# Performance work log

Hardware: AMD Instinct MI355X
Metric: run time of the kernel (lower is better)

## Reference

```python
import jax, jax.numpy as jnp
import numpy as np

B, T, D_IN, D_MODEL = 16, 4096, 256, 128
LN_EPS = 1e-5


def setup_inputs() -> dict:
    key = jax.random.key(0)
    ks = jax.random.split(key, 8)
    s_in = 1.0 / np.sqrt(D_MODEL)  # torch GRU init scale (1/sqrt(hidden))
    x = jax.random.normal(ks[0], (B, T, D_IN), dtype=jnp.float32)
    w_ih = jax.random.uniform(ks[1], (3 * D_MODEL, D_IN), minval=-s_in, maxval=s_in, dtype=jnp.float32)
    w_hh = jax.random.uniform(ks[2], (3 * D_MODEL, D_MODEL), minval=-s_in, maxval=s_in, dtype=jnp.float32)
    b_ih = jax.random.uniform(ks[3], (3 * D_MODEL,), minval=-s_in, maxval=s_in, dtype=jnp.float32)
    b_hh = jax.random.uniform(ks[4], (3 * D_MODEL,), minval=-s_in, maxval=s_in, dtype=jnp.float32)
    w_proj = jax.random.uniform(ks[5], (D_MODEL, D_MODEL), minval=-s_in, maxval=s_in, dtype=jnp.float32)
    b_proj = jax.random.uniform(ks[6], (D_MODEL,), minval=-s_in, maxval=s_in, dtype=jnp.float32)
    gamma = jnp.ones((D_MODEL,), dtype=jnp.float32)
    beta = jnp.zeros((D_MODEL,), dtype=jnp.float32)
    return {"x": x, "w_ih": w_ih, "w_hh": w_hh, "b_ih": b_ih, "b_hh": b_hh,
            "w_proj": w_proj, "b_proj": b_proj, "gamma": gamma, "beta": beta}


def _gru_scan(x, w_ih, w_hh, b_ih, b_hh):
    # x: [B,T,D_in]; precompute input-gate GEMM for all timesteps at once
    gi_all = jnp.einsum('btd,gd->btg', x, w_ih) + b_ih  # [B,T,3H]
    H = w_hh.shape[1]

    def step(h, gi):
        gh = h @ w_hh.T + b_hh                     # [B,3H]
        ir, iz, inn = jnp.split(gi, 3, axis=-1)    # torch gate order: r, z, n
        hr, hz, hn = jnp.split(gh, 3, axis=-1)
        r = jax.nn.sigmoid(ir + hr)
        z = jax.nn.sigmoid(iz + hz)
        n = jnp.tanh(inn + r * hn)
        h_new = (1.0 - z) * n + z * h
        return h_new, h_new

    h0 = jnp.zeros((x.shape[0], H), dtype=x.dtype)
    _, hs = jax.lax.scan(step, h0, jnp.swapaxes(gi_all, 0, 1))  # [T,B,H]
    return jnp.swapaxes(hs, 0, 1)                               # [B,T,H]


def reference(x, w_ih, w_hh, b_ih, b_hh, w_proj, b_proj, gamma, beta):
    out = _gru_scan(x, w_ih, w_hh, b_ih, b_hh)        # GRU output [B,T,H]
    y = out @ w_proj.T + b_proj                        # Linear(d_model, d_model)
    mu = jnp.mean(y, axis=-1, keepdims=True)
    var = jnp.mean(jnp.square(y - mu), axis=-1, keepdims=True)
    return (y - mu) * jax.lax.rsqrt(var + LN_EPS) * gamma + beta
```

## Files before the change

### kernel.cpp

```cpp
#include <hip/hip_runtime.h>
#include <hip/hip_fp16.h>

#define B_   16
#define T_   4096
#define DIN  256
#define H_   128
#define G3   384

#define SC_RZ 1.4426950408889634f
#define SC_N  2.8853900817779268f

typedef _Float16 half2_t __attribute__((ext_vector_type(2)));

__device__ __forceinline__ float fdot2(unsigned int a, unsigned int b, float c) {
#if __has_builtin(__builtin_amdgcn_fdot2)
  return __builtin_amdgcn_fdot2(__builtin_bit_cast(half2_t, a),
                                __builtin_bit_cast(half2_t, b), c, false);
#else
  const __half2 ha = __builtin_bit_cast(__half2, a);
  const __half2 hb = __builtin_bit_cast(__half2, b);
  return c + __half2float(__low2half(ha)) * __half2float(__low2half(hb))
           + __half2float(__high2half(ha)) * __half2float(__high2half(hb));
#endif
}

template <int CTRL>
__device__ __forceinline__ float dpp_xor_add(float x) {
  const int yi = __builtin_amdgcn_mov_dpp(__builtin_bit_cast(int, x),
                                          CTRL, 0xF, 0xF, true);
  return x + __builtin_bit_cast(float, yi);
}

__device__ __forceinline__ unsigned int pack2(float x, float y) {
  __half2 h = __floats2half2_rn(x, y);
  return __builtin_bit_cast(unsigned int, h);
}

__device__ __forceinline__ float fexp2(float x) {
#if __has_builtin(__builtin_amdgcn_exp2f)
  return __builtin_amdgcn_exp2f(x);
#else
  return exp2f(x);
#endif
}
__device__ __forceinline__ float frcp(float x) {
#if __has_builtin(__builtin_amdgcn_rcpf)
  return __builtin_amdgcn_rcpf(x);
#else
  return 1.f / x;
#endif
}

__device__ __forceinline__ void scan_barrier() {
  asm volatile("s_waitcnt lgkmcnt(0)" ::: "memory");
  __builtin_amdgcn_s_barrier();
  asm volatile("" ::: "memory");
}

__device__ __forceinline__ void barrier_lds() {
  asm volatile("s_waitcnt lgkmcnt(0)" ::: "memory");
  __builtin_amdgcn_s_barrier();
  asm volatile("" ::: "memory");
}

__device__ __forceinline__ void wave_lds_fence() {
  asm volatile("s_waitcnt lgkmcnt(0)" ::: "memory");
}

__global__ __launch_bounds__(384, 1) void gi_gemm(
    const float* __restrict__ x, const float* __restrict__ w_ih,
    const float* __restrict__ b_ih, const float* __restrict__ b_hh,
    __half* __restrict__ gi) {
  const int j = threadIdx.x;
  const int rbase = blockIdx.x * 128;

  __half2 wreg[128];
  const float* wrow = w_ih + (size_t)j * DIN;
#pragma unroll
  for (int k = 0; k < 128; ++k) {
    float2 w2 = reinterpret_cast<const float2*>(wrow)[k];
    wreg[k] = __floats2half2_rn(w2.x, w2.y);
  }
  const float bias = b_ih[j] + ((j < 256) ? b_hh[j] : 0.f);
  const __half2 z2h = __floats2half2_rn(0.f, 0.f);

  __shared__ alignas(16) unsigned int xs[16 * 128];

  for (int c = 0; c < 8; ++c) {
    barrier_lds();
    const int row0 = rbase + c * 16;
    for (int i = j; i < 16 * 128; i += 384) {
      const int r = i >> 7, col = i & 127;
      float2 v = reinterpret_cast<const float2*>(x + (size_t)(row0 + r) * DIN)[col];
      xs[i] = pack2(v.x, v.y);
    }
    barrier_lds();
    for (int r = 0; r < 16; ++r) {
      __half2 a0 = z2h, a1 = z2h, a2 = z2h, a3 = z2h;
      const uint4* hp = reinterpret_cast<const uint4*>(xs + r * 128);
#pragma unroll
      for (int k = 0; k < 32; ++k) {
        uint4 hv = hp[k];
        a0 = __hfma2(wreg[4 * k + 0], __builtin_bit_cast(__half2, hv.x), a0);
        a1 = __hfma2(wreg[4 * k + 1], __builtin_bit_cast(__half2, hv.y), a1);
        a2 = __hfma2(wreg[4 * k + 2], __builtin_bit_cast(__half2, hv.z), a2);
        a3 = __hfma2(wreg[4 * k + 3], __builtin_bit_cast(__half2, hv.w), a3);
      }
      const __half2 s2 = __hadd2(__hadd2(a0, a1), __hadd2(a2, a3));
      const float acc = bias + __low2float(s2) + __high2float(s2);
      gi[(size_t)(row0 + r) * G3 + j] = __float2half(acc);
    }
  }
}

__global__ __launch_bounds__(256, 1) void gru_scan(
    const __half* __restrict__ gi, const float* __restrict__ w_hh,
    const float* __restrict__ b_hh, float* __restrict__ out) {
  const int b   = blockIdx.x;
  const int tid = threadIdx.x;
  const int l   = tid & 63;
  const int w   = tid >> 6;
  const int half = l & 1;
  const int c   = w * 32 + (l >> 1);

  __half2 wgt[3][32];
#pragma unroll
  for (int g = 0; g < 3; ++g) {
    const float sg = (g < 2) ? -SC_RZ : -SC_N;
    const float* row = w_hh + (size_t)(g * H_ + c) * H_ + half * 64;
#pragma unroll
    for (int k = 0; k < 32; ++k) {
      float2 a = reinterpret_cast<const float2*>(row)[k];
      wgt[g][k] = __floats2half2_rn(a.x * sg, a.y * sg);
    }
  }
  const float bnS = b_hh[2 * H_ + c] * -SC_N;
  const __half2 initN = __floats2half2_rn((half == 0) ? bnS : 0.f, 0.f);
  const __half2 z2h = __floats2half2_rn(0.f, 0.f);

  __shared__ alignas(16) char hA[288];
  __shared__ alignas(16) char hB[288];
  if (tid < 72) reinterpret_cast<unsigned int*>(hA)[tid] = 0u;

  const int abase = half * 144;
  const int woff  = (c < 64) ? (c * 2) : (144 + (c - 64) * 2);

  const __half* gp = gi + (size_t)b * T_ * G3;
  float* po = out + ((size_t)b * T_) * H_ + c;
  const int o0 = c, o1 = H_ + c, o2 = 2 * H_ + c;

  __half pa0 = gp[o0],          pz0 = gp[o1],          pn0 = gp[o2];
  __half pa1 = gp[G3 + o0],     pz1 = gp[G3 + o1],     pn1 = gp[G3 + o2];
  __half pa2 = gp[2 * G3 + o0], pz2 = gp[2 * G3 + o1], pn2 = gp[2 * G3 + o2];
  __half pa3 = gp[3 * G3 + o0], pz3 = gp[3 * G3 + o1], pn3 = gp[3 * G3 + o2];
  const __half* r0 = gp + 4 * G3;
  const __half* r1 = gp + 5 * G3;
  const __half* r2 = gp + 6 * G3;
  const __half* r3 = gp + 7 * G3;

  float hp = 0.f;
  scan_barrier();

#define STEP(TT, PA, PZ, PN, RB, WB, RP)                                    \
  {                                                                         \
    const float ga = __half2float(PA);                                      \
    const float gz = __half2float(PZ);                                      \
    const float gn = __half2float(PN);                                      \
    if ((TT) + 4 < T_) {               \
      PA = (RP)[o0]; PZ = (RP)[o1]; PN = (RP)[o2];                          \
    }                                                                       \
    RP += 4 * G3;                                                           \
    __half2 aR0 = z2h, aR1 = z2h;                                           \
    __half2 aZ0 = z2h, aZ1 = z2h;                                           \
    __half2 aN0 = initN, aN1 = z2h;                                         \
    _Pragma("unroll")                                                       \
    for (int k = 0; k < 8; ++k) {                                           \
      const uint4 hv = *reinterpret_cast<const uint4*>((RB) + abase + k * 16);\
      const __half2 hx = __builtin_bit_cast(__half2, hv.x);                 \
      const __half2 hy = __builtin_bit_cast(__half2, hv.y);                 \
      const __half2 hz = __builtin_bit_cast(__half2, hv.z);                 \
      const __half2 hw = __builtin_bit_cast(__half2, hv.w);                 \
      aR0 = __hfma2(wgt[0][4 * k + 0], hx, aR0);                            \
      aR1 = __hfma2(wgt[0][4 * k + 1], hy, aR1);                            \
      aR0 = __hfma2(wgt[0][4 * k + 2], hz, aR0);                            \
      aR1 = __hfma2(wgt[0][4 * k + 3], hw, aR1);                            \
      aZ0 = __hfma2(wgt[1][4 * k + 0], hx, aZ0);                            \
      aZ1 = __hfma2(wgt[1][4 * k + 1], hy, aZ1);                            \
      aZ0 = __hfma2(wgt[1][4 * k + 2], hz, aZ0);                            \
      aZ1 = __hfma2(wgt[1][4 * k + 3], hw, aZ1);                            \
      aN0 = __hfma2(wgt[2][4 * k + 0], hx, aN0);                            \
      aN1 = __hfma2(wgt[2][4 * k + 1], hy, aN1);                            \
      aN0 = __hfma2(wgt[2][4 * k + 2], hz, aN0);                            \
      aN1 = __hfma2(wgt[2][4 * k + 3], hw, aN1);                            \
    }                                                                       \
    const __half2 sR = __hadd2(aR0, aR1);                                   \
    const __half2 sZ = __hadd2(aZ0, aZ1);                                   \
    const __half2 sN = __hadd2(aN0, aN1);                                   \
    const float aRs = __low2float(sR) + __high2float(sR);                   \
    const float aZs = __low2float(sZ) + __high2float(sZ);                   \
    const float aNs = __low2float(sN) + __high2float(sN);                   \
    const float fR = dpp_xor_add<0xB1>(aRs);                                \
    const float fZ = dpp_xor_add<0xB1>(aZs);                                \
    const float fN = dpp_xor_add<0xB1>(aNs);                                \
    const float er = fexp2(fmaf(ga, -SC_RZ, fR));                           \
    const float ez = fexp2(fmaf(gz, -SC_RZ, fZ));     \
    const float rg = frcp(1.f + er);                                        \
    const float en = fexp2(fmaf(gn, -SC_N, rg * fN));                       \
    const float num = fmaf(hp, en, hp) + fmaf(-ez, en, ez);                 \
    const float den = fmaf(ez, en, 1.f + ez + en);                          \
    const float h = num * frcp(den);                                        \
    hp = h;                                                                 \
    if (half == 0) {                                                        \
      po[(size_t)(TT) * H_] = h;                                            \
      *reinterpret_cast<__half*>((WB) + woff) = __float2half(h);            \
    }                                                                       \
    scan_barrier();                                                         \
  }

  for (int t = 0; t < T_; t += 4) {
    STEP(t,     pa0, pz0, pn0, hA, hB, r0)
    STEP(t + 1, pa1, pz1, pn1, hB, hA, r1)
    STEP(t + 2, pa2, pz2, pn2, hA, hB, r2)
    STEP(t + 3, pa3, pz3, pn3, hB, hA, r3)
  }
#undef STEP
}

#define PROJ_ROWS 64
__global__ __launch_bounds__(64, 1) void proj_ln(
    float* __restrict__ io, const float* __restrict__ w_proj,
    const float* __restrict__ b_proj, const float* __restrict__ gamma,
    const float* __restrict__ beta) {
  const int lane = threadIdx.x;
  const int row0 = blockIdx.x * PROJ_ROWS;
  const int jA = lane, jB = lane + 64;

  unsigned int wa[64], wb[64];
#pragma unroll
  for (int k = 0; k < 64; ++k) {
    float2 v = reinterpret_cast<const float2*>(w_proj + (size_t)jA * H_)[k];
    wa[k] = pack2(v.x, v.y);
  }
#pragma unroll
  for (int k = 0; k < 64; ++k) {
    float2 v = reinterpret_cast<const float2*>(w_proj + (size_t)jB * H_)[k];
    wb[k] = pack2(v.x, v.y);
  }
  const float bA = b_proj[jA], bB = b_proj[jB];
  const float gmA = gamma[jA], gmB = gamma[jB];
  const float btA = beta[jA], btB = beta[jB];

  __shared__ alignas(16) unsigned int hbuf[64];

  for (int r = 0; r < PROJ_ROWS; ++r) {
    float* rowp = io + (size_t)(row0 + r) * H_;
    float2 v = reinterpret_cast<float2*>(rowp)[lane];
    hbuf[lane] = pack2(v.x, v.y);
    wave_lds_fence();

    float aA = bA, aB = bB;
    const uint4* hp = reinterpret_cast<const uint4*>(hbuf);
#pragma unroll
    for (int k = 0; k < 16; ++k) {
      uint4 hv = hp[k];
      aA = fdot2(wa[4 * k + 0], hv.x, aA);
      aA = fdot2(wa[4 * k + 1], hv.y, aA);
      aA = fdot2(wa[4 * k + 2], hv.z, aA);
      aA = fdot2(wa[4 * k + 3], hv.w, aA);
      aB = fdot2(wb[4 * k + 0], hv.x, aB);
      aB = fdot2(wb[4 * k + 1], hv.y, aB);
      aB = fdot2(wb[4 * k + 2], hv.z, aB);
      aB = fdot2(wb[4 * k + 3], hv.w, aB);
    }

    float s = aA + aB;
    float q = aA * aA + aB * aB;
#pragma unroll
    for (int m = 1; m < 64; m <<= 1) {
      s += __shfl_xor(s, m, 64);
      q += __shfl_xor(q, m, 64);
    }
    const float mu = s * (1.f / 128.f);
    const float var = q * (1.f / 128.f) - mu * mu;
    const float rs = rsqrtf(var + 1e-5f);
    rowp[lane]      = (aA - mu) * rs * gmA + btA;
    rowp[lane + 64] = (aB - mu) * rs * gmB + btB;
    wave_lds_fence();
  }
}

extern "C" void kernel_launch(void* const* d_in, const int* in_sizes, int n_in,
                              void* d_out, int out_size, void* d_ws, size_t ws_size,
                              hipStream_t stream) {
  const float* x      = (const float*)d_in[0];
  const float* w_ih   = (const float*)d_in[1];
  const float* w_hh   = (const float*)d_in[2];
  const float* b_ih   = (const float*)d_in[3];
  const float* b_hh   = (const float*)d_in[4];
  const float* w_proj = (const float*)d_in[5];
  const float* b_proj = (const float*)d_in[6];
  const float* gamma  = (const float*)d_in[7];
  const float* beta   = (const float*)d_in[8];

  float* out = (float*)d_out;
  __half* gi = (__half*)d_ws;

  gi_gemm<<<512, 384, 0, stream>>>(x, w_ih, b_ih, b_hh, gi);
  gru_scan<<<B_, 256, 0, stream>>>(gi, w_hh, b_hh, out);
  proj_ln<<<(B_ * T_) / PROJ_ROWS, 64, 0, stream>>>(out, w_proj, b_proj, gamma, beta);
}
```

Before: 2.250 ms.

## Use MFMA for input-gate GEMM and packed half2 FMA in projection

The input-gate GEMM is rewritten to use 16x16x32 fp16 MFMA instructions, with weight fragments held in registers and x tiles staged through swizzled LDS. The block shape changes to 512 threads over 256 rows. The projection kernel replaces fdot2 with packed half2 FMAs accumulating in fp16, which trades accuracy for throughput. The sequential GRU scan, likely the dominant cost, is unchanged, so total time may move little.

After: 1.922 ms. 14.6% less time.

```diff
diff --git a/kernel.cpp b/kernel.cpp
--- a/kernel.cpp
+++ b/kernel.cpp
@@ -10,19 +10,8 @@
 #define SC_RZ 1.4426950408889634f
 #define SC_N  2.8853900817779268f
 
-typedef _Float16 half2_t __attribute__((ext_vector_type(2)));
-
-__device__ __forceinline__ float fdot2(unsigned int a, unsigned int b, float c) {
-#if __has_builtin(__builtin_amdgcn_fdot2)
-  return __builtin_amdgcn_fdot2(__builtin_bit_cast(half2_t, a),
-                                __builtin_bit_cast(half2_t, b), c, false);
-#else
-  const __half2 ha = __builtin_bit_cast(__half2, a);
-  const __half2 hb = __builtin_bit_cast(__half2, b);
-  return c + __half2float(__low2half(ha)) * __half2float(__low2half(hb))
-           + __half2float(__high2half(ha)) * __half2float(__high2half(hb));
-#endif
-}
+typedef _Float16 half8_t __attribute__((ext_vector_type(8)));
+typedef float f32x4 __attribute__((ext_vector_type(4)));
 
 template <int CTRL>
 __device__ __forceinline__ float dpp_xor_add(float x) {
@@ -67,48 +56,82 @@
   asm volatile("s_waitcnt lgkmcnt(0)" ::: "memory");
 }
 
-__global__ __launch_bounds__(384, 1) void gi_gemm(
+__global__ __launch_bounds__(512, 1) void gi_gemm(
     const float* __restrict__ x, const float* __restrict__ w_ih,
     const float* __restrict__ b_ih, const float* __restrict__ b_hh,
     __half* __restrict__ gi) {
-  const int j = threadIdx.x;
-  const int rbase = blockIdx.x * 128;
-
-  __half2 wreg[128];
-  const float* wrow = w_ih + (size_t)j * DIN;
-#pragma unroll
-  for (int k = 0; k < 128; ++k) {
-    float2 w2 = reinterpret_cast<const float2*>(wrow)[k];
-    wreg[k] = __floats2half2_rn(w2.x, w2.y);
-  }
-  const float bias = b_ih[j] + ((j < 256) ? b_hh[j] : 0.f);
-  const __half2 z2h = __floats2half2_rn(0.f, 0.f);
-
-  __shared__ alignas(16) unsigned int xs[16 * 128];
-
-  for (int c = 0; c < 8; ++c) {
+  const int tid = threadIdx.x;
+  const int l   = tid & 63;
+  const int wv  = tid >> 6;
+  const int l15 = l & 15;
+  const int g4  = l >> 4;
+  const int rbase = blockIdx.x * 256;
+
+  half8_t wf[3][8];
+  float bias[3];
+#pragma unroll
+  for (int ct = 0; ct < 3; ++ct) {
+    const int n = wv * 48 + ct * 16 + l15;
+    const float* wrow = w_ih + (size_t)n * DIN;
+#pragma unroll
+    for (int kt = 0; kt < 8; ++kt) {
+      const float* p = wrow + kt * 32 + g4 * 8;
+      const float4 lo = *reinterpret_cast<const float4*>(p);
+      const float4 hi = *reinterpret_cast<const float4*>(p + 4);
+      half8_t f;
+      f[0] = (_Float16)lo.x; f[1] = (_Float16)lo.y;
+      f[2] = (_Float16)lo.z; f[3] = (_Float16)lo.w;
+      f[4] = (_Float16)hi.x; f[5] = (_Float16)hi.y;
+      f[6] = (_Float16)hi.z; f[7] = (_Float16)hi.w;
+      wf[ct][kt] = f;
+    }
+    bias[ct] = b_ih[n] + ((n < 256) ? b_hh[n] : 0.f);
+  }
+
+  __shared__ alignas(16) char xbuf[16 * 512];
+
+  const int srow = tid >> 5;
+  const int kseg = tid & 31;
+  const int wofs = srow * 512 + ((kseg * 16) ^ ((srow & 7) << 4));
+
+  int aoff[8];
+#pragma unroll
+  for (int kt = 0; kt < 8; ++kt)
+    aoff[kt] = l15 * 512 + ((kt * 64 + g4 * 16) ^ ((l15 & 7) << 4));
+
+  for (int s = 0; s < 16; ++s) {
     barrier_lds();
-    const int row0 = rbase + c * 16;
-    for (int i = j; i < 16 * 128; i += 384) {
-      const int r = i >> 7, col = i & 127;
-      float2 v = reinterpret_cast<const float2*>(x + (size_t)(row0 + r) * DIN)[col];
-      xs[i] = pack2(v.x, v.y);
+    {
+      const float* src = x + (size_t)(rbase + s * 16 + srow) * DIN + kseg * 8;
+      const float4 lo = *reinterpret_cast<const float4*>(src);
+      const float4 hi = *reinterpret_cast<const float4*>(src + 4);
+      half8_t f;
+      f[0] = (_Float16)lo.x; f[1] = (_Float16)lo.y;
+      f[2] = (_Float16)lo.z; f[3] = (_Float16)lo.w;
+      f[4] = (_Float16)hi.x; f[5] = (_Float16)hi.y;
+      f[6] = (_Float16)hi.z; f[7] = (_Float16)hi.w;
+      *reinterpret_cast<half8_t*>(xbuf + wofs) = f;
     }
     barrier_lds();
-    for (int r = 0; r < 16; ++r) {
-      __half2 a0 = z2h, a1 = z2h, a2 = z2h, a3 = z2h;
-      const uint4* hp = reinterpret_cast<const uint4*>(xs + r * 128);
-#pragma unroll
-      for (int k = 0; k < 32; ++k) {
-        uint4 hv = hp[k];
-        a0 = __hfma2(wreg[4 * k + 0], __builtin_bit_cast(__half2, hv.x), a0);
-        a1 = __hfma2(wreg[4 * k + 1], __builtin_bit_cast(__half2, hv.y), a1);
-        a2 = __hfma2(wreg[4 * k + 2], __builtin_bit_cast(__half2, hv.z), a2);
-        a3 = __hfma2(wreg[4 * k + 3], __builtin_bit_cast(__half2, hv.w), a3);
-      }
-      const __half2 s2 = __hadd2(__hadd2(a0, a1), __hadd2(a2, a3));
-      const float acc = bias + __low2float(s2) + __high2float(s2);
-      gi[(size_t)(row0 + r) * G3 + j] = __float2half(acc);
+
+    f32x4 acc0 = {bias[0], bias[0], bias[0], bias[0]};
+    f32x4 acc1 = {bias[1], bias[1], bias[1], bias[1]};
+    f32x4 acc2 = {bias[2], bias[2], bias[2], bias[2]};
+#pragma unroll
+    for (int kt = 0; kt < 8; ++kt) {
+      const half8_t a = *reinterpret_cast<const half8_t*>(xbuf + aoff[kt]);
+      acc0 = __builtin_amdgcn_mfma_f32_16x16x32_f16(a, wf[0][kt], acc0, 0, 0, 0);
+      acc1 = __builtin_amdgcn_mfma_f32_16x16x32_f16(a, wf[1][kt], acc1, 0, 0, 0);
+      acc2 = __builtin_amdgcn_mfma_f32_16x16x32_f16(a, wf[2][kt], acc2, 0, 0, 0);
+    }
+
+    const size_t r0 = (size_t)(rbase + s * 16 + g4 * 4);
+#pragma unroll
+    for (int i = 0; i < 4; ++i) {
+      __half* dst = gi + (r0 + i) * G3 + wv * 48 + l15;
+      dst[0]  = __float2half(acc0[i]);
+      dst[16] = __float2half(acc1[i]);
+      dst[32] = __float2half(acc2[i]);
     }
   }
 }
@@ -166,7 +189,7 @@
     const float ga = __half2float(PA);                                      \
     const float gz = __half2float(PZ);                                      \
     const float gn = __half2float(PN);                                      \
-    if ((TT) + 4 < T_) {               \
+    if ((TT) + 4 < T_) {                                                    \
       PA = (RP)[o0]; PZ = (RP)[o1]; PN = (RP)[o2];                          \
     }                                                                       \
     RP += 4 * G3;                                                           \
@@ -203,7 +226,7 @@
     const float fZ = dpp_xor_add<0xB1>(aZs);                                \
     const float fN = dpp_xor_add<0xB1>(aNs);                                \
     const float er = fexp2(fmaf(ga, -SC_RZ, fR));                           \
-    const float ez = fexp2(fmaf(gz, -SC_RZ, fZ));     \
+    const float ez = fexp2(fmaf(gz, -SC_RZ, fZ));                           \
     const float rg = frcp(1.f + er);                                        \
     const float en = fexp2(fmaf(gn, -SC_N, rg * fN));                       \
     const float num = fmaf(hp, en, hp) + fmaf(-ez, en, ez);                 \
@@ -235,20 +258,21 @@
   const int row0 = blockIdx.x * PROJ_ROWS;
   const int jA = lane, jB = lane + 64;
 
-  unsigned int wa[64], wb[64];
+  __half2 wa2[64], wb2[64];
 #pragma unroll
   for (int k = 0; k < 64; ++k) {
     float2 v = reinterpret_cast<const float2*>(w_proj + (size_t)jA * H_)[k];
-    wa[k] = pack2(v.x, v.y);
+    wa2[k] = __floats2half2_rn(v.x, v.y);
   }
 #pragma unroll
   for (int k = 0; k < 64; ++k) {
     float2 v = reinterpret_cast<const float2*>(w_proj + (size_t)jB * H_)[k];
-    wb[k] = pack2(v.x, v.y);
+    wb2[k] = __floats2half2_rn(v.x, v.y);
   }
   const float bA = b_proj[jA], bB = b_proj[jB];
   const float gmA = gamma[jA], gmB = gamma[jB];
   const float btA = beta[jA], btB = beta[jB];
+  const __half2 z2h = __floats2half2_rn(0.f, 0.f);
 
   __shared__ alignas(16) unsigned int hbuf[64];
 
@@ -258,20 +282,29 @@
     hbuf[lane] = pack2(v.x, v.y);
     wave_lds_fence();
 
-    float aA = bA, aB = bB;
+    __half2 A0 = z2h, A1 = z2h, A2 = z2h, A3 = z2h;
+    __half2 B0 = z2h, B1 = z2h, B2 = z2h, B3 = z2h;
     const uint4* hp = reinterpret_cast<const uint4*>(hbuf);
 #pragma unroll
     for (int k = 0; k < 16; ++k) {
-      uint4 hv = hp[k];
-      aA = fdot2(wa[4 * k + 0], hv.x, aA);
-      aA = fdot2(wa[4 * k + 1], hv.y, aA);
-      aA = fdot2(wa[4 * k + 2], hv.z, aA);
-      aA = fdot2(wa[4 * k + 3], hv.w, aA);
-      aB = fdot2(wb[4 * k + 0], hv.x, aB);
-      aB = fdot2(wb[4 * k + 1], hv.y, aB);
-      aB = fdot2(wb[4 * k + 2], hv.z, aB);
-      aB = fdot2(wb[4 * k + 3], hv.w, aB);
-    }
+      const uint4 hv = hp[k];
+      const __half2 hx = __builtin_bit_cast(__half2, hv.x);
+      const __half2 hy = __builtin_bit_cast(__half2, hv.y);
+      const __half2 hz = __builtin_bit_cast(__half2, hv.z);
+      const __half2 hw = __builtin_bit_cast(__half2, hv.w);
+      A0 = __hfma2(wa2[4 * k + 0], hx, A0);
+      A1 = __hfma2(wa2[4 * k + 1], hy, A1);
+      A2 = __hfma2(wa2[4 * k + 2], hz, A2);
+      A3 = __hfma2(wa2[4 * k + 3], hw, A3);
+      B0 = __hfma2(wb2[4 * k + 0], hx, B0);
+      B1 = __hfma2(wb2[4 * k + 1], hy, B1);
+      B2 = __hfma2(wb2[4 * k + 2], hz, B2);
+      B3 = __hfma2(wb2[4 * k + 3], hw, B3);
+    }
+    const __half2 sA = __hadd2(__hadd2(A0, A1), __hadd2(A2, A3));
+    const __half2 sB = __hadd2(__hadd2(B0, B1), __hadd2(B2, B3));
+    const float aA = bA + __low2float(sA) + __high2float(sA);
+    const float aB = bB + __low2float(sB) + __high2float(sB);
 
     float s = aA + aB;
     float q = aA * aA + aB * aB;
@@ -305,7 +338,7 @@
   float* out = (float*)d_out;
   __half* gi = (__half*)d_ws;
 
-  gi_gemm<<<512, 384, 0, stream>>>(x, w_ih, b_ih, b_hh, gi);
+  gi_gemm<<<256, 512, 0, stream>>>(x, w_ih, b_ih, b_hh, gi);
   gru_scan<<<B_, 256, 0, stream>>>(gi, w_hh, b_hh, out);
   proj_ln<<<(B_ * T_) / PROJ_ROWS, 64, 0, stream>>>(out, w_proj, b_proj, gamma, beta);
 }
```
